# Optimization experiments

Measured on AMD Instinct MI355X. Metric: run time of the kernel, lower is better.

The kernel has to match this reference:

```python
import jax, jax.numpy as jnp
import numpy as np

TEMPERATURE = 0.07
EPS = 1e-12  # F.normalize eps


def _l2_normalize(x):
    # matches torch F.normalize(dim=1): x / max(||x||, eps)
    n = jnp.linalg.norm(x, axis=1, keepdims=True)
    return x / jnp.maximum(n, EPS)


def setup_inputs() -> dict:
    key = jax.random.key(0)
    k1, k2 = jax.random.split(key)
    N, Z = 4096, 256
    z1 = jax.random.normal(k1, (N, Z), dtype=jnp.float32)
    z2 = jax.random.normal(k2, (N, Z), dtype=jnp.float32)
    return {"z1": z1, "z2": z2}


def reference(z1, z2):
    N = z1.shape[0]
    z1n = _l2_normalize(z1)
    z2n = _l2_normalize(z2)
    reps = jnp.concatenate([z1n, z2n], axis=0)          # [2N, Z]
    sim = reps @ reps.T                                  # cosine sim (rows unit-norm)
    # positives: sim[i, i+N] for i<N and sim[i, i-N] for i>=N
    pos = jnp.concatenate([jnp.diagonal(sim, offset=N),
                           jnp.diagonal(sim, offset=-N)])  # [2N]
    # The row logits are {positive} U {all sims except self and positive},
    # i.e. all entries except the self-similarity diagonal.
    inv_t = 1.0 / TEMPERATURE
    twoN = 2 * N
    diag_mask = jnp.eye(twoN, dtype=bool)
    logits = jnp.where(diag_mask, -jnp.inf, sim * inv_t)   # [2N, 2N]
    lse = jax.nn.logsumexp(logits, axis=1)                 # [2N]
    # cross_entropy with label at the positive: -pos/T + lse, sum / 2N
    loss = jnp.mean(lse - pos * inv_t)
    return loss
```

## Files before the change

### kernel.cpp

```cpp
#include <hip/hip_runtime.h>
#include <hip/hip_bf16.h>

#define N_ROWS 4096
#define TWO_N  8192
#define ZDIM   256
#define INV_T  (1.0f/0.07f)
#define EXP_SCALE (INV_T * 1.44269504088896340736f)

typedef __attribute__((ext_vector_type(4))) float f32x4;

__device__ __forceinline__ void async_load16(const void* g, void* lds_uniform_base) {
  __builtin_amdgcn_global_load_lds(
      (const __attribute__((address_space(1))) void*)g,
      (__attribute__((address_space(3))) void*)lds_uniform_base, 16, 0, 0);
}

__device__ __forceinline__ unsigned char f32_to_e4m3(float x) {
  unsigned int u = __float_as_uint(x);
  const unsigned int s = u >> 31;
  unsigned int a = u & 0x7FFFFFFFu;
  if (a > 0x43E00000u) a = 0x43E00000u;
  const float f = __uint_as_float(a);
  unsigned int out;
  if (a < (121u << 23)) {
    const int m = (int)rintf(f * 512.0f);
    out = (unsigned int)m;
  } else {
    const unsigned int r = a + 0x7FFFFu + ((a >> 20) & 1u);
    const unsigned int e8 = (r >> 23) - 120u;
    out = (e8 << 3) | ((r >> 20) & 7u);
  }
  return (unsigned char)(out | (s << 7));
}

__global__ __launch_bounds__(256) void normalize_kernel(
    const float* __restrict__ z1, const float* __restrict__ z2,
    unsigned char* __restrict__ reps, float* __restrict__ pos,
    float* __restrict__ out) {
  const int lane = threadIdx.x & 63;
  const int wave = threadIdx.x >> 6;
  const int r = blockIdx.x * 4 + wave;
  const float4 a = ((const float4*)(z1 + (size_t)r * ZDIM))[lane];
  const float4 b = ((const float4*)(z2 + (size_t)r * ZDIM))[lane];
  float s1 = a.x*a.x + a.y*a.y + a.z*a.z + a.w*a.w;
  float s2 = b.x*b.x + b.y*b.y + b.z*b.z + b.w*b.w;
  float s3 = a.x*b.x + a.y*b.y + a.z*b.z + a.w*b.w;
  #pragma unroll
  for (int m = 1; m < 64; m <<= 1) {
    s1 += __shfl_xor(s1, m, 64);
    s2 += __shfl_xor(s2, m, 64);
    s3 += __shfl_xor(s3, m, 64);
  }
  const float inv1 = 1.0f / fmaxf(sqrtf(s1), 1e-12f);
  const float inv2 = 1.0f / fmaxf(sqrtf(s2), 1e-12f);
  uchar4 pa, pb;
  pa.x = f32_to_e4m3(a.x * inv1); pa.y = f32_to_e4m3(a.y * inv1);
  pa.z = f32_to_e4m3(a.z * inv1); pa.w = f32_to_e4m3(a.w * inv1);
  pb.x = f32_to_e4m3(b.x * inv2); pb.y = f32_to_e4m3(b.y * inv2);
  pb.z = f32_to_e4m3(b.z * inv2); pb.w = f32_to_e4m3(b.w * inv2);
  ((uchar4*)(reps + (size_t)r * ZDIM))[lane] = pa;
  ((uchar4*)(reps + (size_t)(r + N_ROWS) * ZDIM))[lane] = pb;
  if (lane == 0) {
    pos[r] = s3 * inv1 * inv2;
    if (r == 0) out[0] = INV_T;
  }
}

__global__ __launch_bounds__(256, 2) void simsum_kernel(
    const unsigned char* __restrict__ reps,
    float* __restrict__ rowscratch,
    float* __restrict__ colscratch) {
  __shared__ __align__(16) unsigned char Alds[128 * 256];

  const int tid  = threadIdx.x;
  const int lane = tid & 63;
  const int wave = tid >> 6;
  const int wm = wave >> 1, wn = wave & 1;
  const int quad = lane >> 4;
  const int l16  = lane & 15;
  const int itile = blockIdx.x;
  const int chunk = blockIdx.y;
  const int rowBase = itile * 128;
  const char* gbase = (const char*)reps;

  {
    const int r0 = tid >> 4;
    const int src = (tid & 8) | ((tid ^ (tid >> 4)) & 7);
    const char* g0 = gbase + (rowBase + r0) * ZDIM + src * 16;
    char* l0 = (char*)Alds + (wave << 10);
    #pragma unroll
    for (int p = 0; p < 8; ++p)
      async_load16(g0 + p * 16 * ZDIM, l0 + p * 4096);
  }

  int doff[5];
  int nd;
  if (chunk == 0) {
    doff[0] = 0; doff[1] = 1; doff[2] = 2; doff[3] = 3; doff[4] = 32;
    nd = (itile < 32) ? 5 : 4;
  } else {
    doff[0] = chunk * 4; doff[1] = chunk * 4 + 1;
    doff[2] = chunk * 4 + 2; doff[3] = chunk * 4 + 3;
    doff[4] = 0;
    nd = 4;
  }
  const int Q = nd * 2;

#define PREF(q_, buf_) do {                                                     \
    const int t_ = (q_) >> 1, c_ = (q_) & 1;                                    \
    const int jt_ = (itile + doff[t_]) & 63;                                    \
    const char* bp_ = gbase + (size_t)(jt_ * 128 + wn * 64 + l16) * ZDIM        \
                      + c_ * 128 + quad * 8;                                    \
    _Pragma("unroll")                                                           \
    for (int ni_ = 0; ni_ < 4; ++ni_)                                           \
      _Pragma("unroll")                                                         \
      for (int s_ = 0; s_ < 4; ++s_)                                            \
        buf_[ni_ * 4 + s_] = *(const long*)(bp_ + ni_ * 16 * ZDIM + s_ * 32);   \
  } while (0)

#define KSTEPS(c_, buf_) do {                                                   \
    _Pragma("unroll")                                                           \
    for (int ws_ = 0; ws_ < 4; ++ws_) {                                         \
      const int o_ = (c_) * 16 + ws_ * 4 + quad;                                \
      const int k16_ = o_ >> 1, h_ = (o_ & 1) * 8;                              \
      long afrag_[4];                                                           \
      _Pragma("unroll")                                                         \
      for (int mi_ = 0; mi_ < 4; ++mi_) {                                       \
        const int m_ = wm * 64 + mi_ * 16 + l16;                                \
        const int sw_ = (k16_ & 8) | ((k16_ ^ m_) & 7);                         \
        afrag_[mi_] = *(const long*)((const char*)Alds + m_ * 256 + sw_ * 16 + h_); \
      }                                                                         \
      _Pragma("unroll")                                                         \
      for (int mi_ = 0; mi_ < 4; ++mi_)                                         \
        _Pragma("unroll")                                                       \
        for (int ni_ = 0; ni_ < 4; ++ni_)                                       \
          acc[mi_][ni_] = __builtin_amdgcn_mfma_f32_16x16x32_fp8_fp8(           \
              afrag_[mi_], buf_[ni_ * 4 + ws_], acc[mi_][ni_], 0, 0, 0);        \
    }                                                                           \
  } while (0)

  float rowpart[16];
  #pragma unroll
  for (int i = 0; i < 16; ++i) rowpart[i] = 0.0f;
  const f32x4 zero4 = {0.0f, 0.0f, 0.0f, 0.0f};

  long b0[16], b1[16];
  f32x4 acc[4][4];

  PREF(0, b0);
  __syncthreads();

  for (int q = 0; q < Q; q += 2) {
    if (q + 1 < Q) PREF(q + 1, b1);
    #pragma unroll
    for (int mi = 0; mi < 4; ++mi)
      #pragma unroll
      for (int ni = 0; ni < 4; ++ni) acc[mi][ni] = zero4;
    KSTEPS(0, b0);

    if (q + 2 < Q) PREF(q + 2, b0);
    KSTEPS(1, b1);

    const int t = q >> 1;
    const int d = doff[t];
    const int jtile = (itile + d) & 63;
    const bool diag = (d == 0);
    float colpart[4] = {0.0f, 0.0f, 0.0f, 0.0f};
    #pragma unroll
    for (int mi = 0; mi < 4; ++mi)
      #pragma unroll
      for (int r = 0; r < 4; ++r) {
        const int grow = rowBase + wm * 64 + mi * 16 + quad * 4 + r;
        float s = 0.0f;
        #pragma unroll
        for (int ni = 0; ni < 4; ++ni) {
          const int gcol = jtile * 128 + wn * 64 + ni * 16 + l16;
          const float e = exp2f((acc[mi][ni][r] - 1.0f) * EXP_SCALE);
          if (!diag || grow != gcol) s += e;
          colpart[ni] += e;
        }
        rowpart[mi * 4 + r] += s;
      }
    if (!diag) {
      #pragma unroll
      for (int ni = 0; ni < 4; ++ni) {
        float v = colpart[ni];
        v += __shfl_xor(v, 16, 64);
        v += __shfl_xor(v, 32, 64);
        if (quad == 0)
          colscratch[(((jtile * 32) + (d - 1)) * 2 + wm) * 128 + wn * 64 + ni * 16 + l16] = v;
      }
    }
  }
#undef PREF
#undef KSTEPS

  #pragma unroll
  for (int i = 0; i < 16; ++i) {
    float v = rowpart[i];
    v += __shfl_xor(v, 1, 64);
    v += __shfl_xor(v, 2, 64);
    v += __shfl_xor(v, 4, 64);
    v += __shfl_xor(v, 8, 64);
    rowpart[i] = v;
  }
  if (l16 == 0) {
    #pragma unroll
    for (int mi = 0; mi < 4; ++mi)
      #pragma unroll
      for (int r = 0; r < 4; ++r)
        rowscratch[((itile * 8 + chunk) * 2 + wn) * 128 + wm * 64 + mi * 16 + quad * 4 + r]
            = rowpart[mi * 4 + r];
  }
}

__global__ __launch_bounds__(256) void reduce_kernel(
    const float* __restrict__ rowscratch, const float* __restrict__ colscratch,
    const float* __restrict__ pos, float* __restrict__ out) {
  const int j = blockIdx.x;
  const int tid = threadIdx.x;
  float v = 0.0f;
  if (tid < 128) {
    float s = 0.0f;
    #pragma unroll
    for (int c = 0; c < 8; ++c)
      #pragma unroll
      for (int w = 0; w < 2; ++w)
        s += rowscratch[((j * 8 + c) * 2 + w) * 128 + tid];
    const int ns = (j < 32) ? 31 : 32;
    for (int si = 0; si < ns; ++si)
      #pragma unroll
      for (int w = 0; w < 2; ++w)
        s += colscratch[((j * 32 + si) * 2 + w) * 128 + tid];
    v = logf(s) * (1.0f / (float)TWO_N);
  } else if (tid < 192) {
    v = -pos[j * 64 + (tid - 128)] * (INV_T / (float)N_ROWS);
  }
  #pragma unroll
  for (int m = 1; m < 64; m <<= 1) v += __shfl_xor(v, m, 64);
  __shared__ float red[4];
  if ((tid & 63) == 0) red[tid >> 6] = v;
  __syncthreads();
  if (tid == 0) atomicAdd(out, red[0] + red[1] + red[2] + red[3]);
}

extern "C" void kernel_launch(void* const* d_in, const int* in_sizes, int n_in,
                              void* d_out, int out_size, void* d_ws, size_t ws_size,
                              hipStream_t stream) {
  const float* z1 = (const float*)d_in[0];
  const float* z2 = (const float*)d_in[1];
  char* ws = (char*)d_ws;
  unsigned char* reps = (unsigned char*)ws;
  size_t off = (size_t)TWO_N * ZDIM;
  float* pos = (float*)(ws + off);        off += N_ROWS * 4;
  float* rowscratch = (float*)(ws + off); off += 64 * 8 * 2 * 128 * 4;
  float* colscratch = (float*)(ws + off); off += 64 * 32 * 2 * 128 * 4;

  normalize_kernel<<<1024, 256, 0, stream>>>(z1, z2, reps, pos, (float*)d_out);
  simsum_kernel<<<dim3(64, 8), 256, 0, stream>>>(reps, rowscratch, colscratch);
  reduce_kernel<<<64, 256, 0, stream>>>(rowscratch, colscratch, pos, (float*)d_out);
}
```

Measured before the change: 110.5 us.

## Stage B tiles through double-buffered LDS with async loads and double the grid

New measurement: 104.1 us. 1.06x faster.

```diff
diff --git a/kernel.cpp b/kernel.cpp
--- a/kernel.cpp
+++ b/kernel.cpp
@@ -66,11 +66,12 @@
   }
 }
 
-__global__ __launch_bounds__(256, 2) void simsum_kernel(
+__global__ __launch_bounds__(256, 3) void simsum_kernel(
     const unsigned char* __restrict__ reps,
     float* __restrict__ rowscratch,
     float* __restrict__ colscratch) {
   __shared__ __align__(16) unsigned char Alds[128 * 256];
+  __shared__ __align__(16) unsigned char Blds[2][128 * 64];
 
   const int tid  = threadIdx.x;
   const int lane = tid & 63;
@@ -93,49 +94,27 @@
       async_load16(g0 + p * 16 * ZDIM, l0 + p * 4096);
   }
 
-  int doff[5];
+  int doff[3];
   int nd;
   if (chunk == 0) {
-    doff[0] = 0; doff[1] = 1; doff[2] = 2; doff[3] = 3; doff[4] = 32;
-    nd = (itile < 32) ? 5 : 4;
+    doff[0] = 0; doff[1] = 1; doff[2] = 32;
+    nd = (itile < 32) ? 3 : 2;
   } else {
-    doff[0] = chunk * 4; doff[1] = chunk * 4 + 1;
-    doff[2] = chunk * 4 + 2; doff[3] = chunk * 4 + 3;
-    doff[4] = 0;
-    nd = 4;
-  }
-  const int Q = nd * 2;
-
-#define PREF(q_, buf_) do {                                                     \
-    const int t_ = (q_) >> 1, c_ = (q_) & 1;                                    \
+    doff[0] = 2 * chunk; doff[1] = 2 * chunk + 1; doff[2] = 0;
+    nd = 2;
+  }
+  const int Q = nd * 4;
+
+#define STAGE_B(q_) do {                                                        \
+    const int t_ = (q_) >> 2, c4_ = (q_) & 3;                                   \
     const int jt_ = (itile + doff[t_]) & 63;                                    \
-    const char* bp_ = gbase + (size_t)(jt_ * 128 + wn * 64 + l16) * ZDIM        \
-                      + c_ * 128 + quad * 8;                                    \
     _Pragma("unroll")                                                           \
-    for (int ni_ = 0; ni_ < 4; ++ni_)                                           \
-      _Pragma("unroll")                                                         \
-      for (int s_ = 0; s_ < 4; ++s_)                                            \
-        buf_[ni_ * 4 + s_] = *(const long*)(bp_ + ni_ * 16 * ZDIM + s_ * 32);   \
-  } while (0)
-
-#define KSTEPS(c_, buf_) do {                                                   \
-    _Pragma("unroll")                                                           \
-    for (int ws_ = 0; ws_ < 4; ++ws_) {                                         \
-      const int o_ = (c_) * 16 + ws_ * 4 + quad;                                \
-      const int k16_ = o_ >> 1, h_ = (o_ & 1) * 8;                              \
-      long afrag_[4];                                                           \
-      _Pragma("unroll")                                                         \
-      for (int mi_ = 0; mi_ < 4; ++mi_) {                                       \
-        const int m_ = wm * 64 + mi_ * 16 + l16;                                \
-        const int sw_ = (k16_ & 8) | ((k16_ ^ m_) & 7);                         \
-        afrag_[mi_] = *(const long*)((const char*)Alds + m_ * 256 + sw_ * 16 + h_); \
-      }                                                                         \
-      _Pragma("unroll")                                                         \
-      for (int mi_ = 0; mi_ < 4; ++mi_)                                         \
-        _Pragma("unroll")                                                       \
-        for (int ni_ = 0; ni_ < 4; ++ni_)                                       \
-          acc[mi_][ni_] = __builtin_amdgcn_mfma_f32_16x16x32_fp8_fp8(           \
-              afrag_[mi_], buf_[ni_ * 4 + ws_], acc[mi_][ni_], 0, 0, 0);        \
+    for (int p_ = 0; p_ < 2; ++p_) {                                            \
+      const int c_ = p_ * 256 + (wave << 6) + lane;                             \
+      const int row_ = c_ >> 2, sl_ = c_ & 3;                                   \
+      const int g_ = sl_ ^ (row_ & 3);                                          \
+      async_load16(gbase + (size_t)(jt_ * 128 + row_) * ZDIM + c4_ * 64 + g_ * 16, \
+                   (char*)Blds[(q_) & 1] + p_ * 4096 + (wave << 10));           \
     }                                                                           \
   } while (0)
 
@@ -144,56 +123,82 @@
   for (int i = 0; i < 16; ++i) rowpart[i] = 0.0f;
   const f32x4 zero4 = {0.0f, 0.0f, 0.0f, 0.0f};
 
-  long b0[16], b1[16];
+  STAGE_B(0);
+  __syncthreads();
+
   f32x4 acc[4][4];
-
-  PREF(0, b0);
-  __syncthreads();
-
-  for (int q = 0; q < Q; q += 2) {
-    if (q + 1 < Q) PREF(q + 1, b1);
-    #pragma unroll
-    for (int mi = 0; mi < 4; ++mi)
-      #pragma unroll
-      for (int ni = 0; ni < 4; ++ni) acc[mi][ni] = zero4;
-    KSTEPS(0, b0);
-
-    if (q + 2 < Q) PREF(q + 2, b0);
-    KSTEPS(1, b1);
-
-    const int t = q >> 1;
+  for (int q = 0; q < Q; ++q) {
+    if (q + 1 < Q) STAGE_B(q + 1);
+    const int t = q >> 2, c4 = q & 3;
     const int d = doff[t];
     const int jtile = (itile + d) & 63;
     const bool diag = (d == 0);
-    float colpart[4] = {0.0f, 0.0f, 0.0f, 0.0f};
-    #pragma unroll
-    for (int mi = 0; mi < 4; ++mi)
-      #pragma unroll
-      for (int r = 0; r < 4; ++r) {
-        const int grow = rowBase + wm * 64 + mi * 16 + quad * 4 + r;
-        float s = 0.0f;
+
+    if (c4 == 0) {
+      #pragma unroll
+      for (int mi = 0; mi < 4; ++mi)
+        #pragma unroll
+        for (int ni = 0; ni < 4; ++ni) acc[mi][ni] = zero4;
+    }
+
+    #pragma unroll
+    for (int kk = 0; kk < 2; ++kk) {
+      const int ol = kk * 4 + quad;
+      const int o  = c4 * 8 + ol;
+      const int k16 = o >> 1, half = (o & 1) * 8;
+      const int sl = ol >> 1, halfl = (ol & 1) * 8;
+      long afrag[4], bfrag[4];
+      #pragma unroll
+      for (int mi = 0; mi < 4; ++mi) {
+        const int m = wm * 64 + mi * 16 + l16;
+        const int sw = (k16 & 8) | ((k16 ^ m) & 7);
+        afrag[mi] = *(const long*)((const char*)Alds + m * 256 + sw * 16 + half);
+      }
+      #pragma unroll
+      for (int ni = 0; ni < 4; ++ni) {
+        const int n = wn * 64 + ni * 16 + l16;
+        const int sw = sl ^ (n & 3);
+        bfrag[ni] = *(const long*)((const char*)Blds[q & 1] + n * 64 + sw * 16 + halfl);
+      }
+      #pragma unroll
+      for (int mi = 0; mi < 4; ++mi)
+        #pragma unroll
+        for (int ni = 0; ni < 4; ++ni)
+          acc[mi][ni] = __builtin_amdgcn_mfma_f32_16x16x32_fp8_fp8(
+              afrag[mi], bfrag[ni], acc[mi][ni], 0, 0, 0);
+    }
+
+    if (c4 == 3) {
+      float colpart[4] = {0.0f, 0.0f, 0.0f, 0.0f};
+      #pragma unroll
+      for (int mi = 0; mi < 4; ++mi)
+        #pragma unroll
+        for (int r = 0; r < 4; ++r) {
+          const int grow = rowBase + wm * 64 + mi * 16 + quad * 4 + r;
+          float s = 0.0f;
+          #pragma unroll
+          for (int ni = 0; ni < 4; ++ni) {
+            const int gcol = jtile * 128 + wn * 64 + ni * 16 + l16;
+            const float e = exp2f((acc[mi][ni][r] - 1.0f) * EXP_SCALE);
+            if (!diag || grow != gcol) s += e;
+            colpart[ni] += e;
+          }
+          rowpart[mi * 4 + r] += s;
+        }
+      if (!diag) {
         #pragma unroll
         for (int ni = 0; ni < 4; ++ni) {
-          const int gcol = jtile * 128 + wn * 64 + ni * 16 + l16;
-          const float e = exp2f((acc[mi][ni][r] - 1.0f) * EXP_SCALE);
-          if (!diag || grow != gcol) s += e;
-          colpart[ni] += e;
+          float v = colpart[ni];
+          v += __shfl_xor(v, 16, 64);
+          v += __shfl_xor(v, 32, 64);
+          if (quad == 0)
+            colscratch[(((jtile * 32) + (d - 1)) * 2 + wm) * 128 + wn * 64 + ni * 16 + l16] = v;
         }
-        rowpart[mi * 4 + r] += s;
-      }
-    if (!diag) {
-      #pragma unroll
-      for (int ni = 0; ni < 4; ++ni) {
-        float v = colpart[ni];
-        v += __shfl_xor(v, 16, 64);
-        v += __shfl_xor(v, 32, 64);
-        if (quad == 0)
-          colscratch[(((jtile * 32) + (d - 1)) * 2 + wm) * 128 + wn * 64 + ni * 16 + l16] = v;
       }
     }
-  }
-#undef PREF
-#undef KSTEPS
+    __syncthreads();
+  }
+#undef STAGE_B
 
   #pragma unroll
   for (int i = 0; i < 16; ++i) {
@@ -209,7 +214,7 @@
     for (int mi = 0; mi < 4; ++mi)
       #pragma unroll
       for (int r = 0; r < 4; ++r)
-        rowscratch[((itile * 8 + chunk) * 2 + wn) * 128 + wm * 64 + mi * 16 + quad * 4 + r]
+        rowscratch[((itile * 16 + chunk) * 2 + wn) * 128 + wm * 64 + mi * 16 + quad * 4 + r]
             = rowpart[mi * 4 + r];
   }
 }
@@ -223,10 +228,10 @@
   if (tid < 128) {
     float s = 0.0f;
     #pragma unroll
-    for (int c = 0; c < 8; ++c)
+    for (int c = 0; c < 16; ++c)
       #pragma unroll
       for (int w = 0; w < 2; ++w)
-        s += rowscratch[((j * 8 + c) * 2 + w) * 128 + tid];
+        s += rowscratch[((j * 16 + c) * 2 + w) * 128 + tid];
     const int ns = (j < 32) ? 31 : 32;
     for (int si = 0; si < ns; ++si)
       #pragma unroll
@@ -253,10 +258,10 @@
   unsigned char* reps = (unsigned char*)ws;
   size_t off = (size_t)TWO_N * ZDIM;
   float* pos = (float*)(ws + off);        off += N_ROWS * 4;
-  float* rowscratch = (float*)(ws + off); off += 64 * 8 * 2 * 128 * 4;
+  float* rowscratch = (float*)(ws + off); off += 64 * 16 * 2 * 128 * 4;
   float* colscratch = (float*)(ws + off); off += 64 * 32 * 2 * 128 * 4;
 
   normalize_kernel<<<1024, 256, 0, stream>>>(z1, z2, reps, pos, (float*)d_out);
-  simsum_kernel<<<dim3(64, 8), 256, 0, stream>>>(reps, rowscratch, colscratch);
+  simsum_kernel<<<dim3(64, 16), 256, 0, stream>>>(reps, rowscratch, colscratch);
   reduce_kernel<<<64, 256, 0, stream>>>(rowscratch, colscratch, pos, (float*)d_out);
 }
```
